# Kernel optimization log

Hardware: AMD Instinct MI355X
Metric: run time of the kernel (lower is better)

Reference implementation:

```python
import jax, jax.numpy as jnp
import numpy as np

B, S, DIN, DOUT = 4, 2048, 4096, 4096

def setup_inputs() -> dict:
    key = jax.random.key(0)
    k1, k2, k3 = jax.random.split(key, 3)
    inputs = jax.random.normal(k1, (B, S, DIN), dtype=jnp.float32)
    # int8 quantized weight stored as int8, simulated per-channel symmetric quant
    weight = jax.random.randint(k2, (DOUT, DIN), -127, 127, dtype=jnp.int32).astype(jnp.int8)
    weight_scaler = jax.random.uniform(k3, (DOUT,), dtype=jnp.float32) * 0.02
    return {"inputs": inputs, "weight": weight, "weight_scaler": weight_scaler}

def reference(inputs, weight, weight_scaler):
    # F.linear(inputs, weight) * weight_scaler
    # int8 weight is upcast for the matmul; per-output-channel dequant scale applied after.
    w = weight.astype(inputs.dtype)            # [DOUT, DIN]
    out = jnp.einsum('bsi,oi->bso', inputs, w) # [B, S, DOUT]
    return out * weight_scaler                 # broadcast over last dim
```

## Files before the change

### kernel.cpp

```cpp
#include <hip/hip_runtime.h>
#include <cstdint>

#define M_DIM 8192
#define N_DIM 4096
#define K_DIM 4096

typedef unsigned short u16;
typedef unsigned int u32;
typedef __attribute__((ext_vector_type(8))) short short8;
typedef __attribute__((ext_vector_type(4))) float floatx4;

#define AS1 __attribute__((address_space(1)))
#define AS3 __attribute__((address_space(3)))

static __device__ __forceinline__ u16 f2bf(float f) {
    u32 x = __float_as_uint(f);
    x += 0x7FFFu + ((x >> 16) & 1u);
    return (u16)(x >> 16);
}

__global__ void cvt_a_kernel(const float4* __restrict__ in, ushort4* __restrict__ out, int n4) {
    int i = blockIdx.x * blockDim.x + threadIdx.x;
    int stride = gridDim.x * blockDim.x;
    for (; i < n4; i += stride) {
        float4 f = in[i];
        ushort4 u;
        u.x = f2bf(f.x); u.y = f2bf(f.y); u.z = f2bf(f.z); u.w = f2bf(f.w);
        out[i] = u;
    }
}

__global__ void cvt_w_kernel(const int4* __restrict__ in, ushort4* __restrict__ out, int n4) {
    int i = blockIdx.x * blockDim.x + threadIdx.x;
    int stride = gridDim.x * blockDim.x;
    for (; i < n4; i += stride) {
        int4 w = in[i];
        ushort4 u;
        u.x = f2bf((float)w.x);
        u.y = f2bf((float)w.y);
        u.z = f2bf((float)w.z);
        u.w = f2bf((float)w.w);
        out[i] = u;
    }
}


#define GLL(s, d) __builtin_amdgcn_global_load_lds((const AS1 u32*)(const void*)(s), \
                                                   (AS3 u32*)(void*)(d), 16, 0, 0)

#define STAGE_A(kt, h, d) do { \
    const u16* s_ = aSrcTh + (size_t)(h) * (128 * K_DIM) + (size_t)(kt) * 64; \
    char* d_ = ldsC + (d) * 65536 + (h) * 16384 + waveOff; \
    GLL(s_, d_); \
    GLL(s_ + 64 * K_DIM, d_ + 8192); \
} while (0)

#define STAGE_B(kt, h, d) do { \
    const u16* s_ = bSrcTh + (size_t)(h) * (128 * K_DIM) + (size_t)(kt) * 64; \
    char* d_ = ldsC + 32768 + (d) * 65536 + (h) * 16384 + waveOff; \
    GLL(s_, d_); \
    GLL(s_ + 64 * K_DIM, d_ + 8192); \
} while (0)

#define RD(off) (*(const short8*)&lds[(off)])
#define MMA(d, a, b) (d) = __builtin_amdgcn_mfma_f32_16x16x32_bf16((a), (b), (d), 0, 0, 0)
#define BAR() __builtin_amdgcn_s_barrier()

#define PH0(bt) do { \
    _Pragma("unroll") for (int mt_ = 0; mt_ < 4; ++mt_) { \
      aF[mt_][0] = RD((bt) * 32768 + aRowOff + mt_ * 1024 + c0); \
      aF[mt_][1] = RD((bt) * 32768 + aRowOff + mt_ * 1024 + c1); \
    } \
    _Pragma("unroll") for (int nt_ = 0; nt_ < 2; ++nt_) { \
      bF1[nt_][0] = RD((bt) * 32768 + 16384 + bRowOff + (2 + nt_) * 1024 + c0); \
      bF1[nt_][1] = RD((bt) * 32768 + 16384 + bRowOff + (2 + nt_) * 1024 + c1); \
    } \
    BAR(); \
    __builtin_amdgcn_s_setprio(1); \
    _Pragma("unroll") for (int mt_ = 0; mt_ < 4; ++mt_) \
      _Pragma("unroll") for (int nt_ = 0; nt_ < 2; ++nt_) { \
        MMA(acc[mt_][nt_], aF[mt_][0], bF0[nt_][0]); \
        MMA(acc[mt_][nt_], aF[mt_][1], bF0[nt_][1]); \
      } \
    __builtin_amdgcn_s_setprio(0); \
    BAR(); \
} while (0)

#define PH1() do { \
    BAR(); \
    __builtin_amdgcn_s_setprio(1); \
    _Pragma("unroll") for (int mt_ = 0; mt_ < 4; ++mt_) \
      _Pragma("unroll") for (int nt_ = 0; nt_ < 2; ++nt_) { \
        MMA(acc[mt_][2 + nt_], aF[mt_][0], bF1[nt_][0]); \
        MMA(acc[mt_][2 + nt_], aF[mt_][1], bF1[nt_][1]); \
      } \
    __builtin_amdgcn_s_setprio(0); \
    BAR(); \
} while (0)

#define PH2(t, bt, doStg, VM) do { \
    asm volatile("s_waitcnt vmcnt(" #VM ")" ::: "memory"); \
    _Pragma("unroll") for (int mt_ = 0; mt_ < 4; ++mt_) { \
      aF[mt_][0] = RD((bt) * 32768 + aRowOff + (4 + mt_) * 1024 + c0); \
      aF[mt_][1] = RD((bt) * 32768 + aRowOff + (4 + mt_) * 1024 + c1); \
    } \
    if (doStg) { STAGE_B((t) + 2, 0, (bt)); STAGE_B((t) + 2, 1, (bt)); } \
    BAR(); \
    __builtin_amdgcn_s_setprio(1); \
    _Pragma("unroll") for (int mt_ = 0; mt_ < 4; ++mt_) \
      _Pragma("unroll") for (int nt_ = 0; nt_ < 2; ++nt_) { \
        MMA(acc[4 + mt_][nt_], aF[mt_][0], bF0[nt_][0]); \
        MMA(acc[4 + mt_][nt_], aF[mt_][1], bF0[nt_][1]); \
      } \
    __builtin_amdgcn_s_setprio(0); \
    BAR(); \
} while (0)

#define PH3(t, bt, doStg, VM) do { \
    _Pragma("unroll") for (int nt_ = 0; nt_ < 2; ++nt_) { \
      bF0[nt_][0] = RD(((bt) ^ 1) * 32768 + 16384 + bRowOff + nt_ * 1024 + c0); \
      bF0[nt_][1] = RD(((bt) ^ 1) * 32768 + 16384 + bRowOff + nt_ * 1024 + c1); \
    } \
    if (doStg) { STAGE_A((t) + 2, 0, (bt)); STAGE_A((t) + 2, 1, (bt)); } \
    asm volatile("s_waitcnt vmcnt(" #VM ")" ::: "memory"); \
    BAR(); \
    __builtin_amdgcn_s_setprio(1); \
    _Pragma("unroll") for (int mt_ = 0; mt_ < 4; ++mt_) \
      _Pragma("unroll") for (int nt_ = 0; nt_ < 2; ++nt_) { \
        MMA(acc[4 + mt_][2 + nt_], aF[mt_][0], bF1[nt_][0]); \
        MMA(acc[4 + mt_][2 + nt_], aF[mt_][1], bF1[nt_][1]); \
      } \
    __builtin_amdgcn_s_setprio(0); \
    BAR(); \
} while (0)

__global__ void __launch_bounds__(512, 2)
gemm_bf16_256(const u16* __restrict__ A, const u16* __restrict__ W,
              const float* __restrict__ scaler, float* __restrict__ out) {
    __shared__ u16 lds[65536];

    const int tid  = threadIdx.x;
    const int wave = tid >> 6;
    const int lane = tid & 63;
    const int r = lane & 15;
    const int q = lane >> 4;
    const int waveM = wave >> 2;
    const int waveN = wave & 3;

    const int mBase = blockIdx.y * 256;
    const int nBase = blockIdx.x * 256;

    const int aRowOff = (waveM * 128 + r) * 64;
    const int bRowOff = (waveN * 64 + r) * 64;
    const int c0 = (q ^ (r & 7)) * 8;
    const int c1 = c0 ^ 32;
    const int waveOff = wave * 1024;
    char* ldsC = (char*)lds;

    const int srow = tid >> 3;
    const int schk = (tid & 7) ^ (srow & 7);
    const u16* aSrcTh = A + (size_t)(mBase + srow) * K_DIM + schk * 8;
    const u16* bSrcTh = W + (size_t)(nBase + srow) * K_DIM + schk * 8;

    short8 aF[4][2], bF0[2][2], bF1[2][2];
    floatx4 acc[8][4] = {};

    STAGE_B(0, 0, 0); STAGE_B(0, 1, 0); STAGE_A(0, 0, 0); STAGE_A(0, 1, 0);
    STAGE_B(1, 0, 1); STAGE_B(1, 1, 1); STAGE_A(1, 0, 1); STAGE_A(1, 1, 1);
    asm volatile("s_waitcnt vmcnt(8)" ::: "memory");
    BAR();
    #pragma unroll
    for (int nt_ = 0; nt_ < 2; ++nt_) {
        bF0[nt_][0] = RD(16384 + bRowOff + nt_ * 1024 + c0);
        bF0[nt_][1] = RD(16384 + bRowOff + nt_ * 1024 + c1);
    }

    #pragma unroll 1
    for (int tt = 0; tt < 31; ++tt) {
        const int t0 = 2 * tt;
        PH0(0); PH1(); PH2(t0, 0, 1, 4); PH3(t0, 0, 1, 8);
        PH0(1); PH1(); PH2(t0 + 1, 1, 1, 4); PH3(t0 + 1, 1, 1, 8);
    }
    PH0(0); PH1(); PH2(62, 0, 0, 4); PH3(62, 0, 0, 0);
    PH0(1); PH1(); PH2(63, 1, 0, 0); PH3(63, 1, 0, 0);

    const int mW = mBase + waveM * 128;
    const int nW = nBase + waveN * 64;
    #pragma unroll
    for (int nt = 0; nt < 4; ++nt) {
        const int n = nW + nt * 16 + r;
        const float s = scaler[n];
        #pragma unroll
        for (int mt = 0; mt < 8; ++mt) {
            const int m0 = mW + mt * 16 + q * 4;
            #pragma unroll
            for (int j = 0; j < 4; ++j)
                out[(size_t)(m0 + j) * N_DIM + n] = acc[mt][nt][j] * s;
        }
    }
}

__global__ void __launch_bounds__(256)
gemm_fallback_kernel(const float* __restrict__ A, const int* __restrict__ W,
                     const float* __restrict__ scaler, float* __restrict__ out) {
    __shared__ float As[64][33];
    __shared__ float Ws[64][33];
    const int tx = threadIdx.x & 15, ty = threadIdx.x >> 4;
    const int mBase = blockIdx.y * 64, nBase = blockIdx.x * 64;
    float acc[4][4] = {};
    for (int kt = 0; kt < K_DIM; kt += 32) {
        for (int i = threadIdx.x; i < 64 * 32; i += 256) {
            int rr = i >> 5, cc = i & 31;
            As[rr][cc] = A[(size_t)(mBase + rr) * K_DIM + kt + cc];
            Ws[rr][cc] = (float)W[(size_t)(nBase + rr) * K_DIM + kt + cc];
        }
        __syncthreads();
        for (int kk = 0; kk < 32; ++kk) {
            float av[4], bv[4];
#pragma unroll
            for (int i = 0; i < 4; ++i) av[i] = As[ty * 4 + i][kk];
#pragma unroll
            for (int j = 0; j < 4; ++j) bv[j] = Ws[tx * 4 + j][kk];
#pragma unroll
            for (int i = 0; i < 4; ++i)
#pragma unroll
                for (int j = 0; j < 4; ++j) acc[i][j] += av[i] * bv[j];
        }
        __syncthreads();
    }
#pragma unroll
    for (int i = 0; i < 4; ++i)
#pragma unroll
        for (int j = 0; j < 4; ++j) {
            int m = mBase + ty * 4 + i, n = nBase + tx * 4 + j;
            out[(size_t)m * N_DIM + n] = acc[i][j] * scaler[n];
        }
}

extern "C" void kernel_launch(void* const* d_in, const int* in_sizes, int n_in,
                              void* d_out, int out_size, void* d_ws, size_t ws_size,
                              hipStream_t stream) {
    const float* A      = (const float*)d_in[0];
    const int*   W32    = (const int*)d_in[1];
    const float* scaler = (const float*)d_in[2];
    float* out          = (float*)d_out;

    const size_t needA = (size_t)M_DIM * K_DIM * sizeof(u16);
    const size_t needW = (size_t)N_DIM * K_DIM * sizeof(u16);

    if (ws_size >= needA + needW) {
        u16* Abf = (u16*)d_ws;
        u16* Wbf = (u16*)((char*)d_ws + needA);
        cvt_a_kernel<<<4096, 256, 0, stream>>>((const float4*)A, (ushort4*)Abf, M_DIM * K_DIM / 4);
        cvt_w_kernel<<<2048, 256, 0, stream>>>((const int4*)W32, (ushort4*)Wbf, N_DIM * K_DIM / 4);
        dim3 grid(N_DIM / 256, M_DIM / 256);
        gemm_bf16_256<<<grid, 512, 0, stream>>>(Abf, Wbf, scaler, out);
    } else {
        dim3 grid(N_DIM / 64, M_DIM / 64);
        gemm_fallback_kernel<<<grid, 256, 0, stream>>>(A, W32, scaler, out);
    }
}
```

Measured before the change: 486.2 us.

## Switch GEMM to 32x32x16 bf16 MFMA tiles and add workgroup swizzle

Replaces the 16x16x32 MFMA tiling with 32x32x16 instructions, restructuring fragment loads, LDS read offsets, the accumulator layout and the output store mapping. Larger MFMA tiles cut the number of LDS fragment reads and instructions per FLOP. It also remaps block IDs with a swizzle so neighbouring workgroups share A/B tiles in L2. The new read pattern may cause different LDS bank conflicts, and the 64-float accumulators keep register pressure high.

```diff
diff --git a/kernel.cpp b/kernel.cpp
--- a/kernel.cpp
+++ b/kernel.cpp
@@ -8,7 +8,7 @@
 typedef unsigned short u16;
 typedef unsigned int u32;
 typedef __attribute__((ext_vector_type(8))) short short8;
-typedef __attribute__((ext_vector_type(4))) float floatx4;
+typedef __attribute__((ext_vector_type(16))) float floatx16;
 
 #define AS1 __attribute__((address_space(1)))
 #define AS3 __attribute__((address_space(3)))
@@ -63,25 +63,20 @@
 } while (0)
 
 #define RD(off) (*(const short8*)&lds[(off)])
-#define MMA(d, a, b) (d) = __builtin_amdgcn_mfma_f32_16x16x32_bf16((a), (b), (d), 0, 0, 0)
+#define MMA32(d, a, b) (d) = __builtin_amdgcn_mfma_f32_32x32x16_bf16((a), (b), (d), 0, 0, 0)
 #define BAR() __builtin_amdgcn_s_barrier()
 
 #define PH0(bt) do { \
-    _Pragma("unroll") for (int mt_ = 0; mt_ < 4; ++mt_) { \
-      aF[mt_][0] = RD((bt) * 32768 + aRowOff + mt_ * 1024 + c0); \
-      aF[mt_][1] = RD((bt) * 32768 + aRowOff + mt_ * 1024 + c1); \
-    } \
-    _Pragma("unroll") for (int nt_ = 0; nt_ < 2; ++nt_) { \
-      bF1[nt_][0] = RD((bt) * 32768 + 16384 + bRowOff + (2 + nt_) * 1024 + c0); \
-      bF1[nt_][1] = RD((bt) * 32768 + 16384 + bRowOff + (2 + nt_) * 1024 + c1); \
-    } \
-    BAR(); \
-    __builtin_amdgcn_s_setprio(1); \
-    _Pragma("unroll") for (int mt_ = 0; mt_ < 4; ++mt_) \
-      _Pragma("unroll") for (int nt_ = 0; nt_ < 2; ++nt_) { \
-        MMA(acc[mt_][nt_], aF[mt_][0], bF0[nt_][0]); \
-        MMA(acc[mt_][nt_], aF[mt_][1], bF0[nt_][1]); \
-      } \
+    _Pragma("unroll") for (int i_ = 0; i_ < 2; ++i_) \
+      _Pragma("unroll") for (int ks_ = 0; ks_ < 4; ++ks_) \
+        aF[i_][ks_] = RD((bt) * 32768 + aRowOff + i_ * 2048 + c32[ks_]); \
+    _Pragma("unroll") for (int ks_ = 0; ks_ < 4; ++ks_) \
+        bF1[ks_] = RD((bt) * 32768 + 16384 + bRowOff + 2048 + c32[ks_]); \
+    BAR(); \
+    __builtin_amdgcn_s_setprio(1); \
+    _Pragma("unroll") for (int ks_ = 0; ks_ < 4; ++ks_) \
+      _Pragma("unroll") for (int i_ = 0; i_ < 2; ++i_) \
+        MMA32(acc[i_][0], aF[i_][ks_], bF0[ks_]); \
     __builtin_amdgcn_s_setprio(0); \
     BAR(); \
 } while (0)
@@ -89,47 +84,38 @@
 #define PH1() do { \
     BAR(); \
     __builtin_amdgcn_s_setprio(1); \
-    _Pragma("unroll") for (int mt_ = 0; mt_ < 4; ++mt_) \
-      _Pragma("unroll") for (int nt_ = 0; nt_ < 2; ++nt_) { \
-        MMA(acc[mt_][2 + nt_], aF[mt_][0], bF1[nt_][0]); \
-        MMA(acc[mt_][2 + nt_], aF[mt_][1], bF1[nt_][1]); \
-      } \
+    _Pragma("unroll") for (int ks_ = 0; ks_ < 4; ++ks_) \
+      _Pragma("unroll") for (int i_ = 0; i_ < 2; ++i_) \
+        MMA32(acc[i_][1], aF[i_][ks_], bF1[ks_]); \
     __builtin_amdgcn_s_setprio(0); \
     BAR(); \
 } while (0)
 
 #define PH2(t, bt, doStg, VM) do { \
     asm volatile("s_waitcnt vmcnt(" #VM ")" ::: "memory"); \
-    _Pragma("unroll") for (int mt_ = 0; mt_ < 4; ++mt_) { \
-      aF[mt_][0] = RD((bt) * 32768 + aRowOff + (4 + mt_) * 1024 + c0); \
-      aF[mt_][1] = RD((bt) * 32768 + aRowOff + (4 + mt_) * 1024 + c1); \
-    } \
+    _Pragma("unroll") for (int i_ = 0; i_ < 2; ++i_) \
+      _Pragma("unroll") for (int ks_ = 0; ks_ < 4; ++ks_) \
+        aF[i_][ks_] = RD((bt) * 32768 + aRowOff + (2 + i_) * 2048 + c32[ks_]); \
     if (doStg) { STAGE_B((t) + 2, 0, (bt)); STAGE_B((t) + 2, 1, (bt)); } \
     BAR(); \
     __builtin_amdgcn_s_setprio(1); \
-    _Pragma("unroll") for (int mt_ = 0; mt_ < 4; ++mt_) \
-      _Pragma("unroll") for (int nt_ = 0; nt_ < 2; ++nt_) { \
-        MMA(acc[4 + mt_][nt_], aF[mt_][0], bF0[nt_][0]); \
-        MMA(acc[4 + mt_][nt_], aF[mt_][1], bF0[nt_][1]); \
-      } \
+    _Pragma("unroll") for (int ks_ = 0; ks_ < 4; ++ks_) \
+      _Pragma("unroll") for (int i_ = 0; i_ < 2; ++i_) \
+        MMA32(acc[2 + i_][0], aF[i_][ks_], bF0[ks_]); \
     __builtin_amdgcn_s_setprio(0); \
     BAR(); \
 } while (0)
 
 #define PH3(t, bt, doStg, VM) do { \
-    _Pragma("unroll") for (int nt_ = 0; nt_ < 2; ++nt_) { \
-      bF0[nt_][0] = RD(((bt) ^ 1) * 32768 + 16384 + bRowOff + nt_ * 1024 + c0); \
-      bF0[nt_][1] = RD(((bt) ^ 1) * 32768 + 16384 + bRowOff + nt_ * 1024 + c1); \
-    } \
+    _Pragma("unroll") for (int ks_ = 0; ks_ < 4; ++ks_) \
+        bF0[ks_] = RD(((bt) ^ 1) * 32768 + 16384 + bRowOff + c32[ks_]); \
     if (doStg) { STAGE_A((t) + 2, 0, (bt)); STAGE_A((t) + 2, 1, (bt)); } \
     asm volatile("s_waitcnt vmcnt(" #VM ")" ::: "memory"); \
     BAR(); \
     __builtin_amdgcn_s_setprio(1); \
-    _Pragma("unroll") for (int mt_ = 0; mt_ < 4; ++mt_) \
-      _Pragma("unroll") for (int nt_ = 0; nt_ < 2; ++nt_) { \
-        MMA(acc[4 + mt_][2 + nt_], aF[mt_][0], bF1[nt_][0]); \
-        MMA(acc[4 + mt_][2 + nt_], aF[mt_][1], bF1[nt_][1]); \
-      } \
+    _Pragma("unroll") for (int ks_ = 0; ks_ < 4; ++ks_) \
+      _Pragma("unroll") for (int i_ = 0; i_ < 2; ++i_) \
+        MMA32(acc[2 + i_][1], aF[i_][ks_], bF1[ks_]); \
     __builtin_amdgcn_s_setprio(0); \
     BAR(); \
 } while (0)
@@ -142,18 +128,21 @@
     const int tid  = threadIdx.x;
     const int wave = tid >> 6;
     const int lane = tid & 63;
-    const int r = lane & 15;
-    const int q = lane >> 4;
+    const int l31 = lane & 31;
+    const int hi  = lane >> 5;
     const int waveM = wave >> 2;
     const int waveN = wave & 3;
 
-    const int mBase = blockIdx.y * 256;
-    const int nBase = blockIdx.x * 256;
-
-    const int aRowOff = (waveM * 128 + r) * 64;
-    const int bRowOff = (waveN * 64 + r) * 64;
-    const int c0 = (q ^ (r & 7)) * 8;
-    const int c1 = c0 ^ 32;
+    const int wgid = blockIdx.y * 16 + blockIdx.x;
+    const int swz  = (wgid & 7) * 64 + (wgid >> 3);
+    const int mBase = (swz >> 4) * 256;
+    const int nBase = (swz & 15) * 256;
+
+    const int aRowOff = (waveM * 128 + l31) * 64;
+    const int bRowOff = (waveN * 64 + l31) * 64;
+    int c32[4];
+    #pragma unroll
+    for (int ks = 0; ks < 4; ++ks) c32[ks] = ((ks * 2 + hi) ^ (lane & 7)) * 8;
     const int waveOff = wave * 1024;
     char* ldsC = (char*)lds;
 
@@ -162,18 +151,15 @@
     const u16* aSrcTh = A + (size_t)(mBase + srow) * K_DIM + schk * 8;
     const u16* bSrcTh = W + (size_t)(nBase + srow) * K_DIM + schk * 8;
 
-    short8 aF[4][2], bF0[2][2], bF1[2][2];
-    floatx4 acc[8][4] = {};
+    short8 aF[2][4], bF0[4], bF1[4];
+    floatx16 acc[4][2] = {};
 
     STAGE_B(0, 0, 0); STAGE_B(0, 1, 0); STAGE_A(0, 0, 0); STAGE_A(0, 1, 0);
     STAGE_B(1, 0, 1); STAGE_B(1, 1, 1); STAGE_A(1, 0, 1); STAGE_A(1, 1, 1);
     asm volatile("s_waitcnt vmcnt(8)" ::: "memory");
     BAR();
     #pragma unroll
-    for (int nt_ = 0; nt_ < 2; ++nt_) {
-        bF0[nt_][0] = RD(16384 + bRowOff + nt_ * 1024 + c0);
-        bF0[nt_][1] = RD(16384 + bRowOff + nt_ * 1024 + c1);
-    }
+    for (int ks = 0; ks < 4; ++ks) bF0[ks] = RD(16384 + bRowOff + c32[ks]);
 
     #pragma unroll 1
     for (int tt = 0; tt < 31; ++tt) {
@@ -187,15 +173,17 @@
     const int mW = mBase + waveM * 128;
     const int nW = nBase + waveN * 64;
     #pragma unroll
-    for (int nt = 0; nt < 4; ++nt) {
-        const int n = nW + nt * 16 + r;
+    for (int nt = 0; nt < 2; ++nt) {
+        const int n = nW + nt * 32 + l31;
         const float s = scaler[n];
         #pragma unroll
-        for (int mt = 0; mt < 8; ++mt) {
-            const int m0 = mW + mt * 16 + q * 4;
+        for (int mt = 0; mt < 4; ++mt) {
+            const int m0 = mW + mt * 32 + 4 * hi;
             #pragma unroll
-            for (int j = 0; j < 4; ++j)
-                out[(size_t)(m0 + j) * N_DIM + n] = acc[mt][nt][j] * s;
+            for (int reg = 0; reg < 16; ++reg) {
+                const int m = m0 + (reg & 3) + 8 * (reg >> 2);
+                out[(size_t)m * N_DIM + n] = acc[mt][nt][reg] * s;
+            }
         }
     }
 }
```

New measurement: 516.6 us. 1.06x slower.
